# Performance work log

Hardware: AMD Instinct MI355X
Metric: run time of the kernel (lower is better)

The kernel has to match this reference:

```python
import jax, jax.numpy as jnp
import numpy as np

NUM_RAYS = 262144  # 512x512 image
NUM_SAMPLES = 64


def setup_inputs() -> dict:
    key = jax.random.key(0)
    k1, k2 = jax.random.split(key)
    rays_o = jax.random.normal(k1, (NUM_RAYS, 3), dtype=jnp.float32) * 0.1
    d = jax.random.normal(k2, (NUM_RAYS, 3), dtype=jnp.float32)
    rays_d = d / jnp.linalg.norm(d, axis=-1, keepdims=True)
    radii = jnp.full((1,), 1.3, dtype=jnp.float32)  # scene_radii buffer
    return {"rays_o": rays_o, "rays_d": rays_d, "radii": radii, "num_samples": NUM_SAMPLES}


def _raymarch_dense(rays_o, rays_d, radii, num_samples):
    # Ray-AABB (cube of half-extent radius) intersection + depth linspace.
    radius = radii[0]
    inv_d = 1.0 / jnp.where(rays_d == 0, jnp.full_like(rays_d, 1e-6), rays_d)
    off_neg = (-radius - rays_o) * inv_d
    off_pos = (radius - rays_o) * inv_d
    near = jnp.max(jnp.minimum(off_neg, off_pos), axis=-1, keepdims=True)  # [N,1]
    far = jnp.min(jnp.maximum(off_neg, off_pos), axis=-1, keepdims=True)   # [N,1]
    t = jnp.linspace(0.0, 1.0, num_samples, dtype=rays_o.dtype)[None]       # [1,S]
    depth = near + (far - near) * t                                         # [N,S]
    # perturb=False path (deterministic)
    samples = (rays_o[:, None, :] + rays_d[:, None, :] * depth[..., None]) / radius  # [N,S,3]
    deltas = jnp.diff(depth, axis=-1, prepend=near)                          # [N,S]
    # Concrete query_mask: occupied = inside unit sphere of normalized grid.
    mask = jnp.linalg.norm(samples, axis=-1) <= 1.0                          # [N,S] bool
    return samples, depth, deltas, mask


def reference(rays_o, rays_d, radii, num_samples):
    n = rays_o.shape[0]
    samples, depth, deltas, mask = _raymarch_dense(rays_o, rays_d, radii, num_samples)
    M = n * num_samples
    mf = mask.reshape(M)
    # Stable compaction: valid entries first, original order preserved (jnp.argsort is stable).
    order = jnp.argsort(jnp.logical_not(mf))
    num_valid = jnp.sum(mf).astype(jnp.int32)
    ridx_full = jnp.repeat(jnp.arange(n, dtype=jnp.int32), num_samples)
    ridx = ridx_full[order]                                  # [M]
    samples_c = samples.reshape(M, 3)[order]                 # [M,3]
    depth_c = depth.reshape(M)[order]                        # [M]
    deltas_c = deltas.reshape(M)[order][:, None]             # [M,1]
    valid = jnp.arange(M) < num_valid                        # padding indicator
    # mark_pack_boundaries: start of each per-ray pack
    boundary = jnp.concatenate([jnp.ones((1,), bool), ridx[1:] != ridx[:-1]]) & valid
    return ridx, samples_c, depth_c, deltas_c, boundary, num_valid
```

## Files before the change

kernel.cpp:

```cpp
#include <hip/hip_runtime.h>

#pragma clang fp contract(off)

namespace {

constexpr int S = 64;
constexpr float DELTA = 1.0f / 63.0f;

constexpr int RPB = 16;
constexpr int Q = RPB * S;
constexpr int LDSF = 7 * Q + 5 * 16;

__device__ __forceinline__ void ray_nearfar(
    float ox, float oy, float oz,
    float dx, float dy, float dz,
    float R, float& nr, float& fr) {
  float ix = 1.0f / ((dx == 0.0f) ? 1e-6f : dx);
  float iy = 1.0f / ((dy == 0.0f) ? 1e-6f : dy);
  float iz = 1.0f / ((dz == 0.0f) ? 1e-6f : dz);
  float mR = -R;
  float ax = (mR - ox) * ix, bx = (R - ox) * ix;
  float ay = (mR - oy) * iy, by = (R - oy) * iy;
  float az = (mR - oz) * iz, bz = (R - oz) * iz;
  nr = fmaxf(fmaxf(fminf(ax, bx), fminf(ay, by)), fminf(az, bz));
  fr = fminf(fminf(fmaxf(ax, bx), fmaxf(ay, by)), fmaxf(az, bz));
}

__global__ __launch_bounds__(256) void k_count(
    const float* __restrict__ ro, const float* __restrict__ rd,
    const float* __restrict__ radii,
    float4* __restrict__ rayinfo,
    int* __restrict__ L, int* __restrict__ blockSums, int N) {
  int r = blockIdx.x * 256 + threadIdx.x;
  int cnt = 0;
  if (r < N) {
    float R = radii[0];
    float ox = ro[3 * r], oy = ro[3 * r + 1], oz = ro[3 * r + 2];
    float dx = rd[3 * r], dy = rd[3 * r + 1], dz = rd[3 * r + 2];
    float nr, fr;
    ray_nearfar(ox, oy, oz, dx, dy, dz, R, nr, fr);
    float f = fr - nr;
    unsigned lo = 0, hi = 0;
    for (int s = 0; s < S; ++s) {
      float dep = nr + f * ((float)s * DELTA);
      float sx = (ox + dx * dep) / R;
      float sy = (oy + dy * dep) / R;
      float sz = (oz + dz * dep) / R;
      float nm = sqrtf((sx * sx + sy * sy) + sz * sz);
      unsigned bit = (nm <= 1.0f) ? 1u : 0u;
      if (s < 32) lo |= bit << s; else hi |= bit << (s - 32);
      cnt += (int)bit;
    }
    rayinfo[r] = make_float4(nr, f, __uint_as_float(lo), __uint_as_float(hi));
  }
  __shared__ int sm[256];
  sm[threadIdx.x] = cnt;
  __syncthreads();
  for (int off = 1; off < 256; off <<= 1) {
    int t = (threadIdx.x >= off) ? sm[threadIdx.x - off] : 0;
    __syncthreads();
    sm[threadIdx.x] += t;
    __syncthreads();
  }
  if (r < N) L[r] = sm[threadIdx.x] - cnt;
  if (threadIdx.x == 255) blockSums[blockIdx.x] = sm[255];
}

__global__ __launch_bounds__(1024) void k_scan(
    const int* __restrict__ blockSums, int* __restrict__ blockOff,
    int* __restrict__ total, float* __restrict__ out_nv, int nb) {
  __shared__ int sm[1024];
  int x = (threadIdx.x < nb) ? blockSums[threadIdx.x] : 0;
  sm[threadIdx.x] = x;
  __syncthreads();
  for (int off = 1; off < 1024; off <<= 1) {
    int t = (threadIdx.x >= off) ? sm[threadIdx.x - off] : 0;
    __syncthreads();
    sm[threadIdx.x] += t;
    __syncthreads();
  }
  if (threadIdx.x < nb) blockOff[threadIdx.x] = sm[threadIdx.x] - x;
  if (threadIdx.x == 1023) {
    *total = sm[1023];
    out_nv[0] = (float)sm[1023];
  }
}

__global__ __launch_bounds__(256) void k_stage(
    const float* __restrict__ ro, const float* __restrict__ rd,
    const float* __restrict__ radii,
    const float4* __restrict__ rayinfo,
    const int* __restrict__ L, const int* __restrict__ blockOff,
    const int* __restrict__ total,
    float* __restrict__ out, int N) {
  __shared__ __align__(16) float buf[LDSF];
  int nwg = gridDim.x;
  int chunk = nwg >> 3;
  int hw = blockIdx.x;
  int bid = (hw & 7) * chunk + (hw >> 3);
  int r0 = bid * RPB;
  int tid = threadIdx.x;
  int nv = *total;
  int V0 = L[r0] + blockOff[r0 >> 8];
  int rB = r0 + RPB;
  int VB = (rB >= N) ? nv : (L[rB] + blockOff[rB >> 8]);
  int cV = VB - V0;
  int cT = Q - cV;
  int TV = r0 * S - V0;
  size_t tail0 = (size_t)nv + (size_t)TV;
  int tmod = (int)(tail0 & 3);

  int Sv[5], St[5];
  {
    int base = 0;
    #pragma unroll
    for (int a = 0; a < 5; ++a) {
      int k = (a == 1) ? 3 : 1;
      int vm = (k * V0) & 3;
      int tm2 = (k == 3) ? ((3 * (int)(tail0 & 3)) & 3) : tmod;
      Sv[a] = base + vm;
      St[a] = ((Sv[a] + k * cV + 3) & ~3) + tm2;
      base += k * Q + 16;
    }
  }

  int rloc = tid >> 4;
  int r = r0 + rloc;
  float R = radii[0];
  float4 info = rayinfo[r];
  float nr = info.x, f = info.y;
  unsigned long long msk =
      ((unsigned long long)__float_as_uint(info.w) << 32) |
      (unsigned long long)__float_as_uint(info.z);
  float ox = ro[3 * r], oy = ro[3 * r + 1], oz = ro[3 * r + 2];
  float dx = rd[3 * r], dy = rd[3 * r + 1], dz = rd[3 * r + 2];
  int Vr = L[r] + blockOff[r >> 8];
  float fr = (float)r;
  #pragma unroll
  for (int j = 0; j < 4; ++j) {
    int s = (tid & 15) + 16 * j;
    bool bit = (msk >> s) & 1ull;
    int below = __popcll(msk & ((1ull << s) - 1ull));
    float dep = nr + f * ((float)s * DELTA);
    float sx = (ox + dx * dep) / R;
    float sy = (oy + dy * dep) / R;
    float sz = (oz + dz * dep) / R;
    float prev = (s == 0) ? nr : (nr + f * ((float)(s - 1) * DELTA));
    float del = dep - prev;
    int idxv = Vr - V0 + below;
    int idxt = (r * S - Vr) - TV + (s - below);
    int i1 = bit ? idxv : idxt;
    buf[(bit ? Sv[0] : St[0]) + i1] = fr;
    int sb = (bit ? Sv[1] : St[1]) + 3 * i1;
    buf[sb] = sx; buf[sb + 1] = sy; buf[sb + 2] = sz;
    buf[(bit ? Sv[2] : St[2]) + i1] = dep;
    buf[(bit ? Sv[3] : St[3]) + i1] = del;
    buf[(bit ? Sv[4] : St[4]) + i1] = (bit && below == 0) ? 1.0f : 0.0f;
  }
  __syncthreads();

  size_t M = (size_t)N * S;
  auto wr = [&](int lds0, size_t g0, int cnt) {
    int a0 = (int)((4 - (g0 & 3)) & 3);
    if (a0 > cnt) a0 = cnt;
    int body = cnt - a0;
    int n4 = body >> 2, rem = body & 3;
    if (tid < a0) out[g0 + tid] = buf[lds0 + tid];
    int l0 = lds0 + a0;
    for (int c = tid; c < n4; c += 256) {
      float4 v = *reinterpret_cast<const float4*>(&buf[l0 + 4 * c]);
      *reinterpret_cast<float4*>(out + g0 + a0 + 4 * (size_t)c) = v;
    }
    if (tid < rem) {
      int e = 4 * n4 + rem - 1 - tid;
      out[g0 + a0 + e] = buf[l0 + e];
    }
  };
  wr(Sv[0], (size_t)V0, cV);
  wr(St[0], tail0, cT);
  wr(Sv[1], M + 3 * (size_t)V0, 3 * cV);
  wr(St[1], M + 3 * tail0, 3 * cT);
  wr(Sv[2], 4 * M + (size_t)V0, cV);
  wr(St[2], 4 * M + tail0, cT);
  wr(Sv[3], 5 * M + (size_t)V0, cV);
  wr(St[3], 5 * M + tail0, cT);
  wr(Sv[4], 6 * M + (size_t)V0, cV);
  wr(St[4], 6 * M + tail0, cT);
}

}

extern "C" void kernel_launch(void* const* d_in, const int* in_sizes, int n_in,
                              void* d_out, int out_size, void* d_ws, size_t ws_size,
                              hipStream_t stream) {
  const float* ro = (const float*)d_in[0];
  const float* rd = (const float*)d_in[1];
  const float* radii = (const float*)d_in[2];
  int N = in_sizes[0] / 3;
  int M = N * S;
  int nbA = (N + 255) / 256;

  float4* rayinfo = (float4*)d_ws;
  int* wsI = (int*)(rayinfo + N);
  int* L = wsI;
  int* blockSums = wsI + N;
  int* blockOff = blockSums + nbA;
  int* total = blockOff + nbA;

  float* out = (float*)d_out;
  float* out_nv = out + (size_t)7 * (size_t)M;

  k_count<<<nbA, 256, 0, stream>>>(ro, rd, radii, rayinfo, L, blockSums, N);
  k_scan<<<1, 1024, 0, stream>>>(blockSums, blockOff, total, out_nv, nbA);
  k_stage<<<N / RPB, 256, 0, stream>>>(ro, rd, radii, rayinfo, L, blockOff,
                                       total, out, N);
}
```

Before: 140.4 us.

## Share LDS offsets across scalar outputs and batch their global stores

Puts the four scalar output arrays (ray index, depth, delta, boundary) in LDS with a common stride, so they share one valid/tail offset, and writes them in a single loop with four float4 stores per iteration. The xyz samples get their own region. The count kernel now compares the squared norm against a threshold one ulp above 1 instead of calling sqrt. The stage kernel uses fma and multiplication by 1/R instead of division, even though fp contract is off, so results can differ from the reference in low bits. These arithmetic changes risk mask and value mismatches at the sphere boundary.

Result: faster. 134.4 us (-4.3%).

```diff
diff --git a/kernel.cpp b/kernel.cpp
--- a/kernel.cpp
+++ b/kernel.cpp
@@ -9,7 +9,9 @@
 
 constexpr int RPB = 16;
 constexpr int Q = RPB * S;
-constexpr int LDSF = 7 * Q + 5 * 16;
+constexpr int LQ = Q + 16;
+constexpr int SB = 4 * LQ;
+constexpr int LDSF = SB + 3 * Q + 16;
 
 __device__ __forceinline__ void ray_nearfar(
     float ox, float oy, float oz,
@@ -33,6 +35,7 @@
     int* __restrict__ L, int* __restrict__ blockSums, int N) {
   int r = blockIdx.x * 256 + threadIdx.x;
   int cnt = 0;
+  const float QLIM = __uint_as_float(0x3F800001u);
   if (r < N) {
     float R = radii[0];
     float ox = ro[3 * r], oy = ro[3 * r + 1], oz = ro[3 * r + 2];
@@ -46,8 +49,8 @@
       float sx = (ox + dx * dep) / R;
       float sy = (oy + dy * dep) / R;
       float sz = (oz + dz * dep) / R;
-      float nm = sqrtf((sx * sx + sy * sy) + sz * sz);
-      unsigned bit = (nm <= 1.0f) ? 1u : 0u;
+      float q = (sx * sx + sy * sy) + sz * sz;
+      unsigned bit = (q <= QLIM) ? 1u : 0u;
       if (s < 32) lo |= bit << s; else hi |= bit << (s - 32);
       cnt += (int)bit;
     }
@@ -108,25 +111,15 @@
   int cT = Q - cV;
   int TV = r0 * S - V0;
   size_t tail0 = (size_t)nv + (size_t)TV;
-  int tmod = (int)(tail0 & 3);
-
-  int Sv[5], St[5];
-  {
-    int base = 0;
-    #pragma unroll
-    for (int a = 0; a < 5; ++a) {
-      int k = (a == 1) ? 3 : 1;
-      int vm = (k * V0) & 3;
-      int tm2 = (k == 3) ? ((3 * (int)(tail0 & 3)) & 3) : tmod;
-      Sv[a] = base + vm;
-      St[a] = ((Sv[a] + k * cV + 3) & ~3) + tm2;
-      base += k * Q + 16;
-    }
-  }
-
-  int rloc = tid >> 4;
-  int r = r0 + rloc;
+
+  int sv = V0 & 3;
+  int st = ((sv + cV + 3) & ~3) + (int)(tail0 & 3);
+  int svS = (3 * V0) & 3;
+  int stS = ((svS + 3 * cV + 3) & ~3) + (int)((3 * tail0) & 3);
+
+  int r = r0 + (tid >> 4);
   float R = radii[0];
+  float invR = 1.0f / R;
   float4 info = rayinfo[r];
   float nr = info.x, f = info.y;
   unsigned long long msk =
@@ -135,57 +128,102 @@
   float ox = ro[3 * r], oy = ro[3 * r + 1], oz = ro[3 * r + 2];
   float dx = rd[3 * r], dy = rd[3 * r + 1], dz = rd[3 * r + 2];
   int Vr = L[r] + blockOff[r >> 8];
-  float fr = (float)r;
+  float fridx = (float)r;
+  int idxvB = Vr - V0;
+  int idxtB = (r * S - Vr) - TV;
   #pragma unroll
   for (int j = 0; j < 4; ++j) {
     int s = (tid & 15) + 16 * j;
     bool bit = (msk >> s) & 1ull;
     int below = __popcll(msk & ((1ull << s) - 1ull));
-    float dep = nr + f * ((float)s * DELTA);
-    float sx = (ox + dx * dep) / R;
-    float sy = (oy + dy * dep) / R;
-    float sz = (oz + dz * dep) / R;
-    float prev = (s == 0) ? nr : (nr + f * ((float)(s - 1) * DELTA));
-    float del = dep - prev;
-    int idxv = Vr - V0 + below;
-    int idxt = (r * S - Vr) - TV + (s - below);
-    int i1 = bit ? idxv : idxt;
-    buf[(bit ? Sv[0] : St[0]) + i1] = fr;
-    int sb = (bit ? Sv[1] : St[1]) + 3 * i1;
-    buf[sb] = sx; buf[sb + 1] = sy; buf[sb + 2] = sz;
-    buf[(bit ? Sv[2] : St[2]) + i1] = dep;
-    buf[(bit ? Sv[3] : St[3]) + i1] = del;
-    buf[(bit ? Sv[4] : St[4]) + i1] = (bit && below == 0) ? 1.0f : 0.0f;
+    float dep = fmaf(f, (float)s * DELTA, nr);
+    float sx = fmaf(dx, dep, ox) * invR;
+    float sy = fmaf(dy, dep, oy) * invR;
+    float sz = fmaf(dz, dep, oz) * invR;
+    float prev = fmaf(f, (float)(s - 1) * DELTA, nr);
+    float del = s ? (dep - prev) : 0.0f;
+    int i1 = bit ? (idxvB + below) : (idxtB + (s - below));
+    int b0 = (bit ? sv : st) + i1;
+    buf[b0] = fridx;
+    buf[b0 + LQ] = dep;
+    buf[b0 + 2 * LQ] = del;
+    buf[b0 + 3 * LQ] = (bit && below == 0) ? 1.0f : 0.0f;
+    int b1 = SB + (bit ? svS : stS) + 3 * i1;
+    buf[b1] = sx; buf[b1 + 1] = sy; buf[b1 + 2] = sz;
   }
   __syncthreads();
 
   size_t M = (size_t)N * S;
-  auto wr = [&](int lds0, size_t g0, int cnt) {
-    int a0 = (int)((4 - (g0 & 3)) & 3);
-    if (a0 > cnt) a0 = cnt;
-    int body = cnt - a0;
-    int n4 = body >> 2, rem = body & 3;
-    if (tid < a0) out[g0 + tid] = buf[lds0 + tid];
-    int l0 = lds0 + a0;
+  const size_t A1 = 4 * M, A2 = 5 * M, A3 = 6 * M;
+
+  {
+    int a0 = (-V0) & 3; if (a0 > cV) a0 = cV;
+    int body = cV - a0, n4 = body >> 2, rem = body & 3;
+    int l0 = sv + a0;
+    size_t g = (size_t)V0 + a0;
     for (int c = tid; c < n4; c += 256) {
-      float4 v = *reinterpret_cast<const float4*>(&buf[l0 + 4 * c]);
-      *reinterpret_cast<float4*>(out + g0 + a0 + 4 * (size_t)c) = v;
+      int l = l0 + 4 * c; size_t gg = g + 4 * (size_t)c;
+      *(float4*)(out + gg)      = *(const float4*)&buf[l];
+      *(float4*)(out + A1 + gg) = *(const float4*)&buf[l + LQ];
+      *(float4*)(out + A2 + gg) = *(const float4*)&buf[l + 2 * LQ];
+      *(float4*)(out + A3 + gg) = *(const float4*)&buf[l + 3 * LQ];
+    }
+    if (tid < a0) {
+      size_t gg = (size_t)V0 + tid; int l = sv + tid;
+      out[gg] = buf[l]; out[A1 + gg] = buf[l + LQ];
+      out[A2 + gg] = buf[l + 2 * LQ]; out[A3 + gg] = buf[l + 3 * LQ];
     }
     if (tid < rem) {
-      int e = 4 * n4 + rem - 1 - tid;
-      out[g0 + a0 + e] = buf[l0 + e];
-    }
-  };
-  wr(Sv[0], (size_t)V0, cV);
-  wr(St[0], tail0, cT);
-  wr(Sv[1], M + 3 * (size_t)V0, 3 * cV);
-  wr(St[1], M + 3 * tail0, 3 * cT);
-  wr(Sv[2], 4 * M + (size_t)V0, cV);
-  wr(St[2], 4 * M + tail0, cT);
-  wr(Sv[3], 5 * M + (size_t)V0, cV);
-  wr(St[3], 5 * M + tail0, cT);
-  wr(Sv[4], 6 * M + (size_t)V0, cV);
-  wr(St[4], 6 * M + tail0, cT);
+      int e = a0 + 4 * n4 + tid;
+      size_t gg = (size_t)V0 + e; int l = sv + e;
+      out[gg] = buf[l]; out[A1 + gg] = buf[l + LQ];
+      out[A2 + gg] = buf[l + 2 * LQ]; out[A3 + gg] = buf[l + 3 * LQ];
+    }
+  }
+  {
+    int a0 = (int)((-tail0) & 3); if (a0 > cT) a0 = cT;
+    int body = cT - a0, n4 = body >> 2, rem = body & 3;
+    int l0 = st + a0;
+    size_t g = tail0 + a0;
+    for (int c = tid; c < n4; c += 256) {
+      int l = l0 + 4 * c; size_t gg = g + 4 * (size_t)c;
+      *(float4*)(out + gg)      = *(const float4*)&buf[l];
+      *(float4*)(out + A1 + gg) = *(const float4*)&buf[l + LQ];
+      *(float4*)(out + A2 + gg) = *(const float4*)&buf[l + 2 * LQ];
+      *(float4*)(out + A3 + gg) = *(const float4*)&buf[l + 3 * LQ];
+    }
+    if (tid < a0) {
+      size_t gg = tail0 + tid; int l = st + tid;
+      out[gg] = buf[l]; out[A1 + gg] = buf[l + LQ];
+      out[A2 + gg] = buf[l + 2 * LQ]; out[A3 + gg] = buf[l + 3 * LQ];
+    }
+    if (tid < rem) {
+      int e = a0 + 4 * n4 + tid;
+      size_t gg = tail0 + e; int l = st + e;
+      out[gg] = buf[l]; out[A1 + gg] = buf[l + LQ];
+      out[A2 + gg] = buf[l + 2 * LQ]; out[A3 + gg] = buf[l + 3 * LQ];
+    }
+  }
+  {
+    size_t g0 = M + 3 * (size_t)V0; int cnt = 3 * cV;
+    int a0 = (int)((-g0) & 3); if (a0 > cnt) a0 = cnt;
+    int body = cnt - a0, n4 = body >> 2, rem = body & 3;
+    int l0 = SB + svS + a0;
+    for (int c = tid; c < n4; c += 256)
+      *(float4*)(out + g0 + a0 + 4 * (size_t)c) = *(const float4*)&buf[l0 + 4 * c];
+    if (tid < a0) out[g0 + tid] = buf[SB + svS + tid];
+    if (tid < rem) { int e = a0 + 4 * n4 + tid; out[g0 + e] = buf[SB + svS + e]; }
+  }
+  {
+    size_t g0 = M + 3 * tail0; int cnt = 3 * cT;
+    int a0 = (int)((-g0) & 3); if (a0 > cnt) a0 = cnt;
+    int body = cnt - a0, n4 = body >> 2, rem = body & 3;
+    int l0 = SB + stS + a0;
+    for (int c = tid; c < n4; c += 256)
+      *(float4*)(out + g0 + a0 + 4 * (size_t)c) = *(const float4*)&buf[l0 + 4 * c];
+    if (tid < a0) out[g0 + tid] = buf[SB + stS + tid];
+    if (tid < rem) { int e = a0 + 4 * n4 + tid; out[g0 + e] = buf[SB + stS + e]; }
+  }
 }
 
 }
```
